# Optimization experiments

Hardware: AMD Instinct MI355X
Metric: run time of the kernel (lower is better)

Reference implementation:

```python
import jax, jax.numpy as jnp
import numpy as np

B, L1, CTX_TXT, C, NH, HD = 2, 4096, 512, 2048, 16, 128
IMG_LEN = 257           # hard-coded image-context length in WanI2VCrossAttentionProcessor
L2 = IMG_LEN + CTX_TXT
EPS = 1e-6


def setup_inputs() -> dict:
    key = jax.random.key(0)
    ks = jax.random.split(key, 16)
    s = 0.02
    w = lambda k: jax.random.normal(k, (C, C), jnp.float32) * s
    bvec = lambda k: jax.random.normal(k, (C,), jnp.float32) * s
    return {
        "x": jax.random.normal(ks[0], (B, L1, C), jnp.float32),
        "context": jax.random.normal(ks[1], (B, L2, C), jnp.float32),
        "context_lens": jax.random.randint(ks[2], (B,), 1, CTX_TXT + 1, jnp.int32),
        "Wq": w(ks[3]), "bq": bvec(ks[4]), "gq": jnp.ones((C,), jnp.float32),
        "Wk": w(ks[5]), "bk": bvec(ks[6]), "gk": jnp.ones((C,), jnp.float32),
        "Wv": w(ks[7]), "bv": bvec(ks[8]),
        "Wki": w(ks[9]), "bki": bvec(ks[10]), "gki": jnp.ones((C,), jnp.float32),
        "Wvi": w(ks[11]), "bvi": bvec(ks[12]),
        "Wo": w(ks[13]), "bo": bvec(ks[14]),
    }


def rms_norm(x, g):
    # RMSNorm over full channel dim (applied before head reshape, as in source)
    return x * jax.lax.rsqrt(jnp.mean(x * x, axis=-1, keepdims=True) + EPS) * g


def attention(q, k, v, key_mask=None):
    # q: [b, Lq, n, d]; k, v: [b, Lk, n, d]
    scale = 1.0 / np.sqrt(HD).astype(np.float32)
    scores = jnp.einsum('bqnd,bknd->bnqk', q, k) * scale
    if key_mask is not None:
        scores = jnp.where(key_mask, scores, jnp.finfo(scores.dtype).min)
    probs = jax.nn.softmax(scores, axis=-1)
    return jnp.einsum('bnqk,bknd->bqnd', probs, v)


def reference(x, context, context_lens, Wq, bq, gq, Wk, bk, gk, Wv, bv,
              Wki, bki, gki, Wvi, bvi, Wo, bo):
    b = x.shape[0]
    ctx_img = context[:, :IMG_LEN]
    ctx_txt = context[:, IMG_LEN:]

    q = rms_norm(x @ Wq + bq, gq).reshape(b, -1, NH, HD)
    k = rms_norm(ctx_txt @ Wk + bk, gk).reshape(b, -1, NH, HD)
    v = (ctx_txt @ Wv + bv).reshape(b, -1, NH, HD)
    k_img = rms_norm(ctx_img @ Wki + bki, gki).reshape(b, -1, NH, HD)
    v_img = (ctx_img @ Wvi + bvi).reshape(b, -1, NH, HD)

    img_x = attention(q, k_img, v_img)  # no k_lens on image branch
    key_mask = (jnp.arange(CTX_TXT)[None, :] < context_lens[:, None])[:, None, None, :]
    txt_x = attention(q, k, v, key_mask)

    out = (txt_x + img_x).reshape(b, -1, NH * HD)
    return out @ Wo + bo
```

## Files before the change

kernel.cpp:

```cpp
#include <hip/hip_runtime.h>

typedef unsigned short u16;
typedef short short8 __attribute__((ext_vector_type(8)));
typedef float f32x4 __attribute__((ext_vector_type(4)));
typedef unsigned short u16x4 __attribute__((ext_vector_type(4)));

__device__ __forceinline__ u16 f2bf(float f) {
  unsigned u = __builtin_bit_cast(unsigned, f);
  u += 0x7fffu + ((u >> 16) & 1u);
  return (u16)(u >> 16);
}
__device__ __forceinline__ float bf2f(u16 s) {
  unsigned u = ((unsigned)s) << 16;
  return __builtin_bit_cast(float, u);
}
__device__ __forceinline__ unsigned cvtpk_bf16(float a, float b) {
  unsigned r;
  asm("v_cvt_pk_bf16_f32 %0, %1, %2" : "=v"(r) : "v"(a), "v"(b));
  return r;
}

#if __has_builtin(__builtin_amdgcn_exp2f)
#define EXP2F(x) __builtin_amdgcn_exp2f(x)
#else
#define EXP2F(x) exp2f(x)
#endif

#define MFMA32(a, b, c) __builtin_amdgcn_mfma_f32_16x16x32_bf16(a, b, c, 0, 0, 0)

#define GLDS16(gp, lp)                                                         \
  __builtin_amdgcn_global_load_lds(                                            \
      (__attribute__((address_space(1))) void*)(gp),                           \
      (__attribute__((address_space(3))) void*)(lp), 16, 0, 0)

__global__ __launch_bounds__(256) void cast_bf16_k(const float* __restrict__ in,
                                                   u16* __restrict__ out, int n4) {
  int i = blockIdx.x * 256 + threadIdx.x;
  if (i >= n4) return;
  float4 v = ((const float4*)in)[i];
  u16x4 o = { f2bf(v.x), f2bf(v.y), f2bf(v.z), f2bf(v.w) };
  ((u16x4*)out)[i] = o;
}

__global__ __launch_bounds__(256) void transw_k(const float* W0, const float* W1,
                                                const float* W2, const float* W3,
                                                const float* W4, const float* W5,
                                                u16* __restrict__ Wt) {
  int z = blockIdx.z;
  const float* W = z == 0 ? W0 : z == 1 ? W1 : z == 2 ? W2 : z == 3 ? W3 : z == 4 ? W4 : W5;
  u16* T = Wt + (size_t)z * 2048 * 2048;
  __shared__ float tile[64][65];
  int k0 = blockIdx.x * 64, n0 = blockIdx.y * 64;
  int c4 = (threadIdx.x & 15) * 4;
  int r = threadIdx.x >> 4;
#pragma unroll
  for (int i = 0; i < 4; ++i) {
    int row = r + i * 16;
    float4 v = *(const float4*)(W + (size_t)(k0 + row) * 2048 + n0 + c4);
    tile[row][c4 + 0] = v.x; tile[row][c4 + 1] = v.y;
    tile[row][c4 + 2] = v.z; tile[row][c4 + 3] = v.w;
  }
  __syncthreads();
#pragma unroll
  for (int i = 0; i < 4; ++i) {
    int nrow = r + i * 16;
    u16x4 o = { f2bf(tile[c4 + 0][nrow]), f2bf(tile[c4 + 1][nrow]),
                f2bf(tile[c4 + 2][nrow]), f2bf(tile[c4 + 3][nrow]) };
    *(u16x4*)(T + (size_t)(n0 + nrow) * 2048 + k0 + c4) = o;
  }
}

struct GemmJob {
  const u16* A; const u16* Bt; const float* bias; void* out;
  int M; int mode; int ldo;
};
struct GemmJobs { GemmJob j[8]; };

__global__ __launch_bounds__(256) void gemm_k(GemmJobs jobs) {
  GemmJob J = jobs.j[blockIdx.z];
  const int m0 = blockIdx.x * 128;
  if (m0 >= J.M) return;
  const int n0 = blockIdx.y * 128;
  __shared__ u16 Asm[128 * 32];
  __shared__ u16 Bsm[128 * 32];
  const int tid = threadIdx.x;
  const int lane = tid & 63;
  const int l15 = lane & 15, quad = lane >> 4;
  const int wave = tid >> 6;
  const int wr = (wave >> 1) * 64, wc = (wave & 1) * 64;
  f32x4 acc[4][4] = {};
  const int g0 = tid, g1 = tid + 256;
  const u16* ag0 = J.A + (size_t)(m0 + (g0 >> 2)) * 2048 + (g0 & 3) * 8;
  const u16* ag1 = J.A + (size_t)(m0 + (g1 >> 2)) * 2048 + (g1 & 3) * 8;
  const u16* bg0 = J.Bt + (size_t)(n0 + (g0 >> 2)) * 2048 + (g0 & 3) * 8;
  const u16* bg1 = J.Bt + (size_t)(n0 + (g1 >> 2)) * 2048 + (g1 & 3) * 8;
  u16* al0 = Asm + g0 * 8; u16* al1 = Asm + g1 * 8;
  u16* bl0 = Bsm + g0 * 8; u16* bl1 = Bsm + g1 * 8;
  for (int k0 = 0; k0 < 2048; k0 += 32) {
    GLDS16(ag0 + k0, al0);
    GLDS16(ag1 + k0, al1);
    GLDS16(bg0 + k0, bl0);
    GLDS16(bg1 + k0, bl1);
    __syncthreads();
    short8 af[4], bf[4];
#pragma unroll
    for (int mi = 0; mi < 4; ++mi)
      af[mi] = *(const short8*)(Asm + (wr + mi * 16 + l15) * 32 + quad * 8);
#pragma unroll
    for (int ni = 0; ni < 4; ++ni)
      bf[ni] = *(const short8*)(Bsm + (wc + ni * 16 + l15) * 32 + quad * 8);
#pragma unroll
    for (int mi = 0; mi < 4; ++mi)
#pragma unroll
      for (int ni = 0; ni < 4; ++ni)
        acc[mi][ni] = __builtin_amdgcn_mfma_f32_16x16x32_bf16(af[mi], bf[ni], acc[mi][ni], 0, 0, 0);
    __syncthreads();
  }
#pragma unroll
  for (int mi = 0; mi < 4; ++mi) {
#pragma unroll
    for (int ni = 0; ni < 4; ++ni) {
      int nn = n0 + wc + ni * 16 + l15;
      float bv = J.bias[nn];
#pragma unroll
      for (int r = 0; r < 4; ++r) {
        int mm = m0 + wr + mi * 16 + quad * 4 + r;
        if (mm >= J.M) continue;
        float v = acc[mi][ni][r] + bv;
        if (J.mode == 0) {
          ((u16*)J.out)[(size_t)mm * J.ldo + nn] = f2bf(v);
        } else if (J.mode == 1) {
          int ml = mm & 31;
          int mp = (mm & ~31) | (((ml >> 2) & 3) * 8 + (ml >> 4) * 4 + (ml & 3));
          ((u16*)J.out)[(size_t)nn * J.ldo + mp] = f2bf(v);
        } else {
          ((float*)J.out)[(size_t)mm * J.ldo + nn] = v;
        }
      }
    }
  }
}

__global__ __launch_bounds__(512, 2) void gemm256_k(const u16* __restrict__ A,
                                                    const u16* __restrict__ Bt,
                                                    const float* __restrict__ bias,
                                                    void* __restrict__ out,
                                                    int mode) {
  const int m0 = blockIdx.x * 256, n0 = blockIdx.y * 256;
  __shared__ u16 lds[2][2][256 * 32];
  const int tid = threadIdx.x, lane = tid & 63;
  const int l15 = lane & 15, quad = lane >> 4;
  const int wave = tid >> 6;
  const int wr = wave >> 2;
  const int wc = wave & 3;
  const int srow = tid >> 2;
  const int sc = ((tid & 3) ^ ((srow >> 1) & 3)) * 8;
  const u16* Ag = A + (size_t)(m0 + srow) * 2048 + sc;
  const u16* Bg = Bt + (size_t)(n0 + srow) * 2048 + sc;
  const int lxor = (l15 >> 1) & 3;
  f32x4 acc[8][4] = {};

  auto stage = [&](int buf, int kt) {
    const size_t ko = (size_t)kt * 32;
    u16* dA = &lds[buf][0][tid * 8];
    u16* dB = &lds[buf][1][tid * 8];
    GLDS16(Ag + ko, dA);
    GLDS16(Ag + (size_t)128 * 2048 + ko, dA + 4096);
    GLDS16(Bg + ko, dB);
    GLDS16(Bg + (size_t)128 * 2048 + ko, dB + 4096);
  };

  stage(0, 0);
  for (int t = 0; t < 64; ++t) {
    const int cb = t & 1;
    __syncthreads();
    if (t + 1 < 64) stage(cb ^ 1, t + 1);
    const u16* Ab = &lds[cb][0][(size_t)wr * 128 * 32];
    const u16* Bb = &lds[cb][1][0];
    short8 bfr[4];
#pragma unroll
    for (int ni = 0; ni < 4; ++ni) {
      const int rn = wc * 64 + ni * 16 + l15;
      bfr[ni] = *(const short8*)(Bb + rn * 32 + ((quad ^ lxor) * 8));
    }
#pragma unroll
    for (int mi = 0; mi < 8; ++mi) {
      const int rm = mi * 16 + l15;
      short8 a = *(const short8*)(Ab + rm * 32 + ((quad ^ lxor) * 8));
      __builtin_amdgcn_s_setprio(1);
#pragma unroll
      for (int ni = 0; ni < 4; ++ni)
        acc[mi][ni] = MFMA32(a, bfr[ni], acc[mi][ni]);
      __builtin_amdgcn_s_setprio(0);
    }
  }
#pragma unroll
  for (int mi = 0; mi < 8; ++mi) {
#pragma unroll
    for (int ni = 0; ni < 4; ++ni) {
      const int nn = n0 + wc * 64 + ni * 16 + l15;
      const float bv = bias[nn];
      const int mm = m0 + wr * 128 + mi * 16 + quad * 4;
      if (mode == 0) {
        u16* op = (u16*)out + (size_t)mm * 2048 + nn;
#pragma unroll
        for (int r = 0; r < 4; ++r) op[(size_t)r * 2048] = f2bf(acc[mi][ni][r] + bv);
      } else {
        float* op = (float*)out + (size_t)mm * 2048 + nn;
#pragma unroll
        for (int r = 0; r < 4; ++r) op[(size_t)r * 2048] = acc[mi][ni][r] + bv;
      }
    }
  }
}

__global__ __launch_bounds__(256) void rmsnorm_k(u16* __restrict__ buf,
                                                 const float* __restrict__ g) {
  const int row = blockIdx.x, tid = threadIdx.x;
  u16* p = buf + (size_t)row * 2048 + tid * 8;
  short8 v = *(short8*)p;
  float x[8]; float s = 0.f;
#pragma unroll
  for (int i = 0; i < 8; ++i) { x[i] = bf2f((u16)v[i]); s += x[i] * x[i]; }
#pragma unroll
  for (int o = 1; o < 64; o <<= 1) s += __shfl_xor(s, o, 64);
  __shared__ float ws4[4];
  if ((tid & 63) == 0) ws4[tid >> 6] = s;
  __syncthreads();
  float tot = ws4[0] + ws4[1] + ws4[2] + ws4[3];
  float scale = rsqrtf(tot * (1.0f / 2048.0f) + 1e-6f);
  const float* gp = g + tid * 8;
  short8 o8;
#pragma unroll
  for (int i = 0; i < 8; ++i) o8[i] = (short)f2bf(x[i] * scale * gp[i]);
  *(short8*)p = o8;
}

__global__ __launch_bounds__(256) void attn_k(const u16* __restrict__ Q,
                                              const u16* __restrict__ Kt,
                                              const u16* __restrict__ Vt,
                                              const u16* __restrict__ Ki,
                                              const u16* __restrict__ Vi,
                                              const int* __restrict__ lens,
                                              u16* __restrict__ out) {
  const int lid = blockIdx.x + 32 * (blockIdx.y + 16 * blockIdx.z);
  const int w = (lid & 7) * 128 + (lid >> 3);
  const int qx = w & 31, hb = w >> 5;
  const int h = hb & 15, b = hb >> 4;

  const int tid = threadIdx.x, lane = tid & 63, wave = tid >> 6;
  const int l15 = lane & 15, quad = lane >> 4;
  const int qbase = qx * 128 + wave * 32;
  const float scale2 = 0.12752358514837517f;
  const float NEGINF = -__builtin_inff();
  __shared__ u16 Ksm[3][32 * 128];
  __shared__ u16 Vsm[3][128 * 32];

  short8 qf[2][4];
#pragma unroll
  for (int h2 = 0; h2 < 2; ++h2) {
    const u16* qb = Q + ((size_t)(b * 4096 + qbase + h2 * 16 + l15)) * 2048 + h * 128 + quad * 8;
#pragma unroll
    for (int kc = 0; kc < 4; ++kc) qf[h2][kc] = *(const short8*)(qb + kc * 32);
  }

  const int krow = tid >> 4;
  const int kcc = ((tid & 15) ^ (krow & 7)) * 8;
  const int vd = tid >> 2;
  const int vcs = ((tid & 3) ^ ((tid >> 3) & 3)) * 8;
  const int kxor = l15 & 7;
  const int vxor = (l15 >> 1) & 3;

  f32x4 accv[2][8];
  u16x4 oimg[2][8];
  float run_m[2], run_l[2];

  auto phase = [&](const u16* Kb, const u16* Vb, int Lv, int ldv) {
    run_m[0] = run_m[1] = NEGINF;
    run_l[0] = run_l[1] = 0.f;
#pragma unroll
    for (int h2 = 0; h2 < 2; ++h2)
#pragma unroll
      for (int dt = 0; dt < 8; ++dt)
#pragma unroll
        for (int r = 0; r < 4; ++r) accv[h2][dt][r] = 0.f;
    const u16* kg0 = Kb + (size_t)krow * 2048 + kcc;
    const u16* kg1 = kg0 + 16 * 2048;
    const u16* vg0 = Vb + (size_t)vd * ldv + vcs;
    const u16* vg1 = vg0 + (size_t)64 * ldv;
    const int ntiles = (Lv + 31) >> 5;
    __builtin_amdgcn_s_barrier();
    {
      GLDS16(kg0, &Ksm[0][tid * 8]);
      GLDS16(kg1, &Ksm[0][2048 + tid * 8]);
      GLDS16(vg0, &Vsm[0][tid * 8]);
      GLDS16(vg1, &Vsm[0][2048 + tid * 8]);
      const size_t k1 = (ntiles > 1) ? 32 : 0;
      GLDS16(kg0 + k1 * 2048, &Ksm[1][tid * 8]);
      GLDS16(kg1 + k1 * 2048, &Ksm[1][2048 + tid * 8]);
      GLDS16(vg0 + k1, &Vsm[1][tid * 8]);
      GLDS16(vg1 + k1, &Vsm[1][2048 + tid * 8]);
    }
    int cb = 0, nb = 2;
    for (int t = 0; t < ntiles; ++t) {
      asm volatile("s_waitcnt vmcnt(4)" ::: "memory");
      __builtin_amdgcn_s_barrier();
      {
        const size_t kn = (size_t)((t + 2 < ntiles) ? (t + 2) * 32 : 0);
        GLDS16(kg0 + kn * 2048, &Ksm[nb][tid * 8]);
        GLDS16(kg1 + kn * 2048, &Ksm[nb][2048 + tid * 8]);
        GLDS16(vg0 + kn, &Vsm[nb][tid * 8]);
        GLDS16(vg1 + kn, &Vsm[nb][2048 + tid * 8]);
      }
      const u16* Ks = Ksm[cb];
      const u16* Vs = Vsm[cb];

      short8 kf0[4], kf1[4];
#pragma unroll
      for (int kc = 0; kc < 4; ++kc) {
        int c0 = ((kc * 4 + quad) ^ kxor) * 8;
        kf0[kc] = *(const short8*)(Ks + l15 * 128 + c0);
        kf1[kc] = *(const short8*)(Ks + (16 + l15) * 128 + c0);
      }
      f32x4 s0[2], s1[2];
#pragma unroll
      for (int h2 = 0; h2 < 2; ++h2)
#pragma unroll
        for (int r = 0; r < 4; ++r) { s0[h2][r] = 0.f; s1[h2][r] = 0.f; }
      __builtin_amdgcn_s_setprio(1);
#pragma unroll
      for (int h2 = 0; h2 < 2; ++h2)
#pragma unroll
        for (int kc = 0; kc < 4; ++kc) {
          s0[h2] = MFMA32(kf0[kc], qf[h2][kc], s0[h2]);
          s1[h2] = MFMA32(kf1[kc], qf[h2][kc], s1[h2]);
        }
      __builtin_amdgcn_s_setprio(0);
      const int kv0 = t * 32;
      if (kv0 + 32 > Lv) {
#pragma unroll
        for (int h2 = 0; h2 < 2; ++h2)
#pragma unroll
          for (int r = 0; r < 4; ++r) {
            const int k0i = kv0 + quad * 4 + r;
            if (k0i >= Lv) s0[h2][r] = NEGINF;
            if (k0i + 16 >= Lv) s1[h2][r] = NEGINF;
          }
      }
      float al[2];
      short8 pf[2];
#pragma unroll
      for (int h2 = 0; h2 < 2; ++h2) {
        float mx = fmaxf(fmaxf(fmaxf(s0[h2][0], s0[h2][1]), fmaxf(s0[h2][2], s0[h2][3])),
                         fmaxf(fmaxf(s1[h2][0], s1[h2][1]), fmaxf(s1[h2][2], s1[h2][3])));
        mx = fmaxf(mx, __shfl_xor(mx, 16, 64));
        mx = fmaxf(mx, __shfl_xor(mx, 32, 64));
        const float nm = fmaxf(run_m[h2], mx);
        al[h2] = EXP2F((run_m[h2] - nm) * scale2);
        run_m[h2] = nm;
        const float nmc = -nm * scale2;
        float p0[4], p1[4], psum = 0.f;
#pragma unroll
        for (int r = 0; r < 4; ++r) {
          p0[r] = EXP2F(__builtin_fmaf(s0[h2][r], scale2, nmc));
          p1[r] = EXP2F(__builtin_fmaf(s1[h2][r], scale2, nmc));
          psum += p0[r] + p1[r];
        }
        run_l[h2] = __builtin_fmaf(run_l[h2], al[h2], psum);
        union { short8 s8; unsigned u[4]; } pp;
        pp.u[0] = cvtpk_bf16(p0[0], p0[1]);
        pp.u[1] = cvtpk_bf16(p0[2], p0[3]);
        pp.u[2] = cvtpk_bf16(p1[0], p1[1]);
        pp.u[3] = cvtpk_bf16(p1[2], p1[3]);
        pf[h2] = pp.s8;
      }
      if (t != 0 && __ballot((al[0] < 1.0f) || (al[1] < 1.0f))) {
#pragma unroll
        for (int h2 = 0; h2 < 2; ++h2)
#pragma unroll
          for (int dt = 0; dt < 8; ++dt)
#pragma unroll
            for (int r = 0; r < 4; ++r) accv[h2][dt][r] *= al[h2];
      }
      __builtin_amdgcn_s_setprio(1);
#pragma unroll
      for (int dt = 0; dt < 8; ++dt) {
        short8 vf = *(const short8*)(Vs + (dt * 16 + l15) * 32 + ((quad ^ vxor) * 8));
        accv[0][dt] = MFMA32(vf, pf[0], accv[0][dt]);
        accv[1][dt] = MFMA32(vf, pf[1], accv[1][dt]);
      }
      __builtin_amdgcn_s_setprio(0);
      cb = (cb == 2) ? 0 : cb + 1;
      nb = (nb == 2) ? 0 : nb + 1;
    }
  };

  const u16* Kb_i = Ki + (size_t)(b * 288) * 2048 + h * 128;
  const u16* Vb_i = Vi + ((size_t)(b * 16 + h) * 128) * 288;
  phase(Kb_i, Vb_i, 257, 288);
#pragma unroll
  for (int h2 = 0; h2 < 2; ++h2) {
    float a = run_l[h2] + __shfl_xor(run_l[h2], 16, 64);
    float lt = a + __shfl_xor(a, 32, 64);
    float inv = 1.0f / lt;
#pragma unroll
    for (int dt = 0; dt < 8; ++dt) {
      u16x4 w2 = { f2bf(accv[h2][dt][0] * inv), f2bf(accv[h2][dt][1] * inv),
                   f2bf(accv[h2][dt][2] * inv), f2bf(accv[h2][dt][3] * inv) };
      oimg[h2][dt] = w2;
    }
  }
  const u16* Kb_t = Kt + (size_t)(b * 512) * 2048 + h * 128;
  const u16* Vb_t = Vt + ((size_t)(b * 16 + h) * 128) * 512;
  phase(Kb_t, Vb_t, lens[b], 512);
#pragma unroll
  for (int h2 = 0; h2 < 2; ++h2) {
    float a = run_l[h2] + __shfl_xor(run_l[h2], 16, 64);
    float lt = a + __shfl_xor(a, 32, 64);
    float inv = 1.0f / lt;
    u16* ob = out + ((size_t)(b * 4096 + qbase + h2 * 16 + l15)) * 2048 + h * 128 + quad * 4;
#pragma unroll
    for (int dt = 0; dt < 8; ++dt) {
      u16x4 w2 = { f2bf(bf2f(oimg[h2][dt][0]) + accv[h2][dt][0] * inv),
                   f2bf(bf2f(oimg[h2][dt][1]) + accv[h2][dt][1] * inv),
                   f2bf(bf2f(oimg[h2][dt][2]) + accv[h2][dt][2] * inv),
                   f2bf(bf2f(oimg[h2][dt][3]) + accv[h2][dt][3] * inv) };
      *(u16x4*)(ob + dt * 16) = w2;
    }
  }
}

extern "C" void kernel_launch(void* const* d_in, const int* in_sizes, int n_in,
                              void* d_out, int out_size, void* d_ws, size_t ws_size,
                              hipStream_t stream) {
  const float* x   = (const float*)d_in[0];
  const float* ctx = (const float*)d_in[1];
  const int* lens  = (const int*)d_in[2];
  const float* Wq  = (const float*)d_in[3];
  const float* bq  = (const float*)d_in[4];
  const float* gq  = (const float*)d_in[5];
  const float* Wk  = (const float*)d_in[6];
  const float* bk  = (const float*)d_in[7];
  const float* gk  = (const float*)d_in[8];
  const float* Wv  = (const float*)d_in[9];
  const float* bv  = (const float*)d_in[10];
  const float* Wki = (const float*)d_in[11];
  const float* bki = (const float*)d_in[12];
  const float* gki = (const float*)d_in[13];
  const float* Wvi = (const float*)d_in[14];
  const float* bvi = (const float*)d_in[15];
  const float* Wo  = (const float*)d_in[16];
  const float* bo  = (const float*)d_in[17];
  float* out = (float*)d_out;

  char* p = (char*)d_ws;
  u16* x_bf   = (u16*)p; p += (size_t)8192 * 2048 * 2;
  u16* ctx_bf = (u16*)p; p += (size_t)2 * 769 * 2048 * 2;
  u16* Wt     = (u16*)p; p += (size_t)6 * 2048 * 2048 * 2;
  u16* Qb     = (u16*)p; p += (size_t)8192 * 2048 * 2;
  u16* Ktxt   = (u16*)p; p += (size_t)2 * 512 * 2048 * 2;
  u16* Vtt    = (u16*)p; p += (size_t)2 * 16 * 128 * 512 * 2;
  u16* Kimg   = (u16*)p; p += (size_t)2 * 288 * 2048 * 2;
  u16* Vti    = (u16*)p; p += (size_t)2 * 16 * 128 * 288 * 2;
  u16* attn_o = x_bf;

  cast_bf16_k<<<16384, 256, 0, stream>>>(x, x_bf, 8192 * 2048 / 4);
  cast_bf16_k<<<3076, 256, 0, stream>>>(ctx, ctx_bf, 2 * 769 * 2048 / 4);
  transw_k<<<dim3(32, 32, 6), 256, 0, stream>>>(Wq, Wk, Wv, Wki, Wvi, Wo, Wt);

  gemm256_k<<<dim3(32, 8), 512, 0, stream>>>(x_bf, Wt + 0ull * 4194304, bq, Qb, 0);

  GemmJobs jc = {};
  for (int b = 0; b < 2; ++b) {
    const u16* txtA = ctx_bf + (size_t)(b * 769 + 257) * 2048;
    const u16* imgA = ctx_bf + (size_t)(b * 769) * 2048;
    jc.j[0 + b] = { txtA, Wt + 1ull * 4194304, bk,  Ktxt + (size_t)b * 512 * 2048, 512, 0, 2048 };
    jc.j[2 + b] = { txtA, Wt + 2ull * 4194304, bv,  Vtt  + (size_t)b * 2048 * 512, 512, 1, 512 };
    jc.j[4 + b] = { imgA, Wt + 3ull * 4194304, bki, Kimg + (size_t)b * 288 * 2048, 257, 0, 2048 };
    jc.j[6 + b] = { imgA, Wt + 4ull * 4194304, bvi, Vti  + (size_t)b * 2048 * 288, 257, 1, 288 };
  }
  gemm_k<<<dim3(4, 16, 8), 256, 0, stream>>>(jc);

  rmsnorm_k<<<8192, 256, 0, stream>>>(Qb, gq);
  rmsnorm_k<<<1024, 256, 0, stream>>>(Ktxt, gk);
  rmsnorm_k<<<576, 256, 0, stream>>>(Kimg, gki);

  attn_k<<<dim3(32, 16, 2), 256, 0, stream>>>(Qb, Ktxt, Vtt, Kimg, Vti, lens, attn_o);

  gemm256_k<<<dim3(32, 8), 512, 0, stream>>>(attn_o, Wt + 5ull * 4194304, bo, out, 1);
}
```

Before: 595.1 us.

## Use 512-thread attention blocks with 64-key tiles and double buffering

New measurement: 514.9 us. 1.16x faster.

```diff
diff --git a/kernel.cpp b/kernel.cpp
--- a/kernel.cpp
+++ b/kernel.cpp
@@ -236,25 +236,25 @@
   *(short8*)p = o8;
 }
 
-__global__ __launch_bounds__(256) void attn_k(const u16* __restrict__ Q,
+__global__ __launch_bounds__(512) void attn_k(const u16* __restrict__ Q,
                                               const u16* __restrict__ Kt,
                                               const u16* __restrict__ Vt,
                                               const u16* __restrict__ Ki,
                                               const u16* __restrict__ Vi,
                                               const int* __restrict__ lens,
                                               u16* __restrict__ out) {
-  const int lid = blockIdx.x + 32 * (blockIdx.y + 16 * blockIdx.z);
-  const int w = (lid & 7) * 128 + (lid >> 3);
-  const int qx = w & 31, hb = w >> 5;
+  const int lid = blockIdx.x + 16 * (blockIdx.y + 16 * blockIdx.z);
+  const int w = (lid & 7) * 64 + (lid >> 3);
+  const int qx = w & 15, hb = w >> 4;
   const int h = hb & 15, b = hb >> 4;
 
   const int tid = threadIdx.x, lane = tid & 63, wave = tid >> 6;
   const int l15 = lane & 15, quad = lane >> 4;
-  const int qbase = qx * 128 + wave * 32;
+  const int qbase = qx * 256 + wave * 32;
   const float scale2 = 0.12752358514837517f;
   const float NEGINF = -__builtin_inff();
-  __shared__ u16 Ksm[3][32 * 128];
-  __shared__ u16 Vsm[3][128 * 32];
+  __shared__ u16 Ksm[2][2][32 * 128];
+  __shared__ u16 Vsm[2][2][128 * 32];
 
   short8 qf[2][4];
 #pragma unroll
@@ -267,7 +267,7 @@
   const int krow = tid >> 4;
   const int kcc = ((tid & 15) ^ (krow & 7)) * 8;
   const int vd = tid >> 2;
-  const int vcs = ((tid & 3) ^ ((tid >> 3) & 3)) * 8;
+  const int vcs = ((tid & 3) ^ ((vd >> 1) & 3)) * 8;
   const int kxor = l15 & 7;
   const int vxor = (l15 >> 1) & 3;
 
@@ -275,7 +275,7 @@
   u16x4 oimg[2][8];
   float run_m[2], run_l[2];
 
-  auto phase = [&](const u16* Kb, const u16* Vb, int Lv, int ldv) {
+  auto phase = [&](const u16* Kb, const u16* Vb, int Lv, int LK) {
     run_m[0] = run_m[1] = NEGINF;
     run_l[0] = run_l[1] = 0.f;
 #pragma unroll
@@ -284,95 +284,116 @@
       for (int dt = 0; dt < 8; ++dt)
 #pragma unroll
         for (int r = 0; r < 4; ++r) accv[h2][dt][r] = 0.f;
-    const u16* kg0 = Kb + (size_t)krow * 2048 + kcc;
-    const u16* kg1 = kg0 + 16 * 2048;
-    const u16* vg0 = Vb + (size_t)vd * ldv + vcs;
-    const u16* vg1 = vg0 + (size_t)64 * ldv;
-    const int ntiles = (Lv + 31) >> 5;
-    __builtin_amdgcn_s_barrier();
-    {
-      GLDS16(kg0, &Ksm[0][tid * 8]);
-      GLDS16(kg1, &Ksm[0][2048 + tid * 8]);
-      GLDS16(vg0, &Vsm[0][tid * 8]);
-      GLDS16(vg1, &Vsm[0][2048 + tid * 8]);
-      const size_t k1 = (ntiles > 1) ? 32 : 0;
-      GLDS16(kg0 + k1 * 2048, &Ksm[1][tid * 8]);
-      GLDS16(kg1 + k1 * 2048, &Ksm[1][2048 + tid * 8]);
-      GLDS16(vg0 + k1, &Vsm[1][tid * 8]);
-      GLDS16(vg1 + k1, &Vsm[1][2048 + tid * 8]);
-    }
-    int cb = 0, nb = 2;
+    const u16* kg = Kb + (size_t)krow * 2048 + kcc;
+    const u16* vg = Vb + (size_t)vd * LK + vcs;
+    const int ntiles = (Lv + 63) >> 6;
+    auto stage = [&](int buf, int t) {
+      const int kvA = t * 64;
+      const int sA = (kvA < LK - 32) ? kvA : (LK - 32);
+      const int sB = (kvA + 32 < LK - 32) ? (kvA + 32) : (LK - 32);
+      GLDS16(kg + (size_t)sA * 2048, &Ksm[buf][0][tid * 8]);
+      GLDS16(kg + (size_t)sB * 2048, &Ksm[buf][1][tid * 8]);
+      GLDS16(vg + sA, &Vsm[buf][0][tid * 8]);
+      GLDS16(vg + sB, &Vsm[buf][1][tid * 8]);
+    };
+    stage(0, 0);
+    __syncthreads();
     for (int t = 0; t < ntiles; ++t) {
-      asm volatile("s_waitcnt vmcnt(4)" ::: "memory");
-      __builtin_amdgcn_s_barrier();
+      const int cb = t & 1;
+      if (t + 1 < ntiles) stage(cb ^ 1, t + 1);
+
+      f32x4 s[2][4];
+#pragma unroll
+      for (int h2 = 0; h2 < 2; ++h2)
+#pragma unroll
+        for (int kb = 0; kb < 4; ++kb)
+#pragma unroll
+          for (int r = 0; r < 4; ++r) s[h2][kb][r] = 0.f;
       {
-        const size_t kn = (size_t)((t + 2 < ntiles) ? (t + 2) * 32 : 0);
-        GLDS16(kg0 + kn * 2048, &Ksm[nb][tid * 8]);
-        GLDS16(kg1 + kn * 2048, &Ksm[nb][2048 + tid * 8]);
-        GLDS16(vg0 + kn, &Vsm[nb][tid * 8]);
-        GLDS16(vg1 + kn, &Vsm[nb][2048 + tid * 8]);
-      }
-      const u16* Ks = Ksm[cb];
-      const u16* Vs = Vsm[cb];
-
-      short8 kf0[4], kf1[4];
-#pragma unroll
-      for (int kc = 0; kc < 4; ++kc) {
-        int c0 = ((kc * 4 + quad) ^ kxor) * 8;
-        kf0[kc] = *(const short8*)(Ks + l15 * 128 + c0);
-        kf1[kc] = *(const short8*)(Ks + (16 + l15) * 128 + c0);
-      }
-      f32x4 s0[2], s1[2];
-#pragma unroll
-      for (int h2 = 0; h2 < 2; ++h2)
-#pragma unroll
-        for (int r = 0; r < 4; ++r) { s0[h2][r] = 0.f; s1[h2][r] = 0.f; }
-      __builtin_amdgcn_s_setprio(1);
-#pragma unroll
-      for (int h2 = 0; h2 < 2; ++h2)
+        short8 kA[2][4];
 #pragma unroll
         for (int kc = 0; kc < 4; ++kc) {
-          s0[h2] = MFMA32(kf0[kc], qf[h2][kc], s0[h2]);
-          s1[h2] = MFMA32(kf1[kc], qf[h2][kc], s1[h2]);
+          const int c0 = ((kc * 4 + quad) ^ kxor) * 8;
+          kA[0][kc] = *(const short8*)(&Ksm[cb][0][l15 * 128 + c0]);
+          kA[1][kc] = *(const short8*)(&Ksm[cb][0][(16 + l15) * 128 + c0]);
         }
-      __builtin_amdgcn_s_setprio(0);
-      const int kv0 = t * 32;
-      if (kv0 + 32 > Lv) {
+        __builtin_amdgcn_s_setprio(1);
 #pragma unroll
         for (int h2 = 0; h2 < 2; ++h2)
 #pragma unroll
-          for (int r = 0; r < 4; ++r) {
-            const int k0i = kv0 + quad * 4 + r;
-            if (k0i >= Lv) s0[h2][r] = NEGINF;
-            if (k0i + 16 >= Lv) s1[h2][r] = NEGINF;
+          for (int kc = 0; kc < 4; ++kc) {
+            s[h2][0] = MFMA32(kA[0][kc], qf[h2][kc], s[h2][0]);
+            s[h2][1] = MFMA32(kA[1][kc], qf[h2][kc], s[h2][1]);
           }
-      }
+        __builtin_amdgcn_s_setprio(0);
+      }
+      {
+        short8 kB[2][4];
+#pragma unroll
+        for (int kc = 0; kc < 4; ++kc) {
+          const int c0 = ((kc * 4 + quad) ^ kxor) * 8;
+          kB[0][kc] = *(const short8*)(&Ksm[cb][1][l15 * 128 + c0]);
+          kB[1][kc] = *(const short8*)(&Ksm[cb][1][(16 + l15) * 128 + c0]);
+        }
+        __builtin_amdgcn_s_setprio(1);
+#pragma unroll
+        for (int h2 = 0; h2 < 2; ++h2)
+#pragma unroll
+          for (int kc = 0; kc < 4; ++kc) {
+            s[h2][2] = MFMA32(kB[0][kc], qf[h2][kc], s[h2][2]);
+            s[h2][3] = MFMA32(kB[1][kc], qf[h2][kc], s[h2][3]);
+          }
+        __builtin_amdgcn_s_setprio(0);
+      }
+
+      const int kvA = t * 64;
+      if (kvA + 64 > Lv) {
+#pragma unroll
+        for (int h2 = 0; h2 < 2; ++h2)
+#pragma unroll
+          for (int kb = 0; kb < 4; ++kb)
+#pragma unroll
+            for (int r = 0; r < 4; ++r) {
+              const int ki = kvA + kb * 16 + quad * 4 + r;
+              if (ki >= Lv) s[h2][kb][r] = NEGINF;
+            }
+      }
+
       float al[2];
-      short8 pf[2];
+      short8 pfA[2], pfB[2];
 #pragma unroll
       for (int h2 = 0; h2 < 2; ++h2) {
-        float mx = fmaxf(fmaxf(fmaxf(s0[h2][0], s0[h2][1]), fmaxf(s0[h2][2], s0[h2][3])),
-                         fmaxf(fmaxf(s1[h2][0], s1[h2][1]), fmaxf(s1[h2][2], s1[h2][3])));
+        float m0 = fmaxf(fmaxf(s[h2][0][0], s[h2][0][1]), fmaxf(s[h2][0][2], s[h2][0][3]));
+        float m1 = fmaxf(fmaxf(s[h2][1][0], s[h2][1][1]), fmaxf(s[h2][1][2], s[h2][1][3]));
+        float m2 = fmaxf(fmaxf(s[h2][2][0], s[h2][2][1]), fmaxf(s[h2][2][2], s[h2][2][3]));
+        float m3 = fmaxf(fmaxf(s[h2][3][0], s[h2][3][1]), fmaxf(s[h2][3][2], s[h2][3][3]));
+        float mx = fmaxf(fmaxf(m0, m1), fmaxf(m2, m3));
         mx = fmaxf(mx, __shfl_xor(mx, 16, 64));
         mx = fmaxf(mx, __shfl_xor(mx, 32, 64));
         const float nm = fmaxf(run_m[h2], mx);
         al[h2] = EXP2F((run_m[h2] - nm) * scale2);
         run_m[h2] = nm;
         const float nmc = -nm * scale2;
-        float p0[4], p1[4], psum = 0.f;
-#pragma unroll
-        for (int r = 0; r < 4; ++r) {
-          p0[r] = EXP2F(__builtin_fmaf(s0[h2][r], scale2, nmc));
-          p1[r] = EXP2F(__builtin_fmaf(s1[h2][r], scale2, nmc));
-          psum += p0[r] + p1[r];
-        }
+        float p[4][4], psum = 0.f;
+#pragma unroll
+        for (int kb = 0; kb < 4; ++kb)
+#pragma unroll
+          for (int r = 0; r < 4; ++r) {
+            p[kb][r] = EXP2F(__builtin_fmaf(s[h2][kb][r], scale2, nmc));
+            psum += p[kb][r];
+          }
         run_l[h2] = __builtin_fmaf(run_l[h2], al[h2], psum);
-        union { short8 s8; unsigned u[4]; } pp;
-        pp.u[0] = cvtpk_bf16(p0[0], p0[1]);
-        pp.u[1] = cvtpk_bf16(p0[2], p0[3]);
-        pp.u[2] = cvtpk_bf16(p1[0], p1[1]);
-        pp.u[3] = cvtpk_bf16(p1[2], p1[3]);
-        pf[h2] = pp.s8;
+        union { short8 s8; unsigned u[4]; } pa, pb;
+        pa.u[0] = cvtpk_bf16(p[0][0], p[0][1]);
+        pa.u[1] = cvtpk_bf16(p[0][2], p[0][3]);
+        pa.u[2] = cvtpk_bf16(p[1][0], p[1][1]);
+        pa.u[3] = cvtpk_bf16(p[1][2], p[1][3]);
+        pb.u[0] = cvtpk_bf16(p[2][0], p[2][1]);
+        pb.u[1] = cvtpk_bf16(p[2][2], p[2][3]);
+        pb.u[2] = cvtpk_bf16(p[3][0], p[3][1]);
+        pb.u[3] = cvtpk_bf16(p[3][2], p[3][3]);
+        pfA[h2] = pa.s8;
+        pfB[h2] = pb.s8;
       }
       if (t != 0 && __ballot((al[0] < 1.0f) || (al[1] < 1.0f))) {
 #pragma unroll
@@ -382,16 +403,20 @@
 #pragma unroll
             for (int r = 0; r < 4; ++r) accv[h2][dt][r] *= al[h2];
       }
+
       __builtin_amdgcn_s_setprio(1);
 #pragma unroll
       for (int dt = 0; dt < 8; ++dt) {
-        short8 vf = *(const short8*)(Vs + (dt * 16 + l15) * 32 + ((quad ^ vxor) * 8));
-        accv[0][dt] = MFMA32(vf, pf[0], accv[0][dt]);
-        accv[1][dt] = MFMA32(vf, pf[1], accv[1][dt]);
+        const int vo = (dt * 16 + l15) * 32 + ((quad ^ vxor) * 8);
+        short8 vfA = *(const short8*)(&Vsm[cb][0][vo]);
+        short8 vfB = *(const short8*)(&Vsm[cb][1][vo]);
+        accv[0][dt] = MFMA32(vfA, pfA[0], accv[0][dt]);
+        accv[1][dt] = MFMA32(vfA, pfA[1], accv[1][dt]);
+        accv[0][dt] = MFMA32(vfB, pfB[0], accv[0][dt]);
+        accv[1][dt] = MFMA32(vfB, pfB[1], accv[1][dt]);
       }
       __builtin_amdgcn_s_setprio(0);
-      cb = (cb == 2) ? 0 : cb + 1;
-      nb = (nb == 2) ? 0 : nb + 1;
+      __syncthreads();
     }
   };
 
@@ -485,7 +510,7 @@
   rmsnorm_k<<<1024, 256, 0, stream>>>(Ktxt, gk);
   rmsnorm_k<<<576, 256, 0, stream>>>(Kimg, gki);
 
-  attn_k<<<dim3(32, 16, 2), 256, 0, stream>>>(Qb, Ktxt, Vtt, Kimg, Vti, lens, attn_o);
+  attn_k<<<dim3(16, 16, 2), 512, 0, stream>>>(Qb, Ktxt, Vtt, Kimg, Vti, lens, attn_o);
 
   gemm256_k<<<dim3(32, 8), 512, 0, stream>>>(attn_o, Wt + 5ull * 4194304, bo, out, 1);
 }
```
